# Kernel tuning notes

Hardware: AMD Instinct MI355X
Metric: run time of the kernel (lower is better)

## Reference

```python
import jax, jax.numpy as jnp
import numpy as np
import math

B, S, D_MODEL, N_HEAD, D_HEAD, D_FFN = 1, 2048, 1024, 16, 64, 4096
EPS = 1e-6


def setup_inputs() -> dict:
    key = jax.random.key(0)
    ks = jax.random.split(key, 10)
    scale = 0.02
    x = jax.random.normal(ks[0], (B, S, D_MODEL), dtype=jnp.float32)
    # RoPE frequencies: freqs_cis[s, i] = exp(1j * s * theta_i), theta_i = 10000^{-2i/d_head}
    half = D_HEAD // 2
    inv_freq = 1.0 / (10000.0 ** (jnp.arange(0, half, dtype=jnp.float32) * 2.0 / D_HEAD))
    angles = jnp.arange(S, dtype=jnp.float32)[:, None] * inv_freq[None, :]  # [S, half]
    freqs_cos = jnp.cos(angles)
    freqs_sin = jnp.sin(angles)
    wq = jax.random.normal(ks[1], (D_MODEL, N_HEAD * D_HEAD), dtype=jnp.float32) * scale
    wk = jax.random.normal(ks[2], (D_MODEL, N_HEAD * D_HEAD), dtype=jnp.float32) * scale
    wv = jax.random.normal(ks[3], (D_MODEL, N_HEAD * D_HEAD), dtype=jnp.float32) * scale
    wo = jax.random.normal(ks[4], (N_HEAD * D_HEAD, D_MODEL), dtype=jnp.float32) * scale
    w1 = jax.random.normal(ks[5], (D_MODEL, D_FFN), dtype=jnp.float32) * scale
    w2 = jax.random.normal(ks[6], (D_FFN, D_MODEL), dtype=jnp.float32) * scale
    w3 = jax.random.normal(ks[7], (D_MODEL, D_FFN), dtype=jnp.float32) * scale
    attn_norm_w = jnp.ones((D_MODEL,), dtype=jnp.float32)
    ffn_norm_w = jnp.ones((D_MODEL,), dtype=jnp.float32)
    return {"x": x, "freqs_cos": freqs_cos, "freqs_sin": freqs_sin,
            "wq": wq, "wk": wk, "wv": wv, "wo": wo,
            "w1": w1, "w2": w2, "w3": w3,
            "attn_norm_w": attn_norm_w, "ffn_norm_w": ffn_norm_w}


def _rmsnorm(x, w):
    xf = x.astype(jnp.float32)
    inv = jax.lax.rsqrt(jnp.mean(xf * xf, axis=-1, keepdims=True) + EPS)
    return (xf * inv).astype(x.dtype) * w


def _rope(t, cos, sin):
    # t: [B, S, H, D]; treat last dim as interleaved (even, odd) complex pairs
    b, s, h, d = t.shape
    tr = t.astype(jnp.float32).reshape(b, s, h, d // 2, 2)
    te, to = tr[..., 0], tr[..., 1]
    c = cos[None, :, None, :]
    sn = sin[None, :, None, :]
    out = jnp.stack([te * c - to * sn, te * sn + to * c], axis=-1)
    return out.reshape(b, s, h, d).astype(t.dtype)


def reference(x, freqs_cos, freqs_sin, wq, wk, wv, wo, w1, w2, w3, attn_norm_w, ffn_norm_w):
    bsz, seqlen, _ = x.shape
    # --- attention sub-block ---
    hin = _rmsnorm(x, attn_norm_w)
    q = (hin @ wq).reshape(bsz, seqlen, N_HEAD, D_HEAD)
    k = (hin @ wk).reshape(bsz, seqlen, N_HEAD, D_HEAD)
    v = (hin @ wv).reshape(bsz, seqlen, N_HEAD, D_HEAD)
    q = _rope(q, freqs_cos, freqs_sin)
    k = _rope(k, freqs_cos, freqs_sin)
    # [B, H, S, S] scores, softmax in fp32 (no causal mask in original)
    scores = jnp.einsum('bqhd,bkhd->bhqk', q, k) / math.sqrt(D_HEAD)
    probs = jax.nn.softmax(scores.astype(jnp.float32), axis=-1).astype(q.dtype)
    attn = jnp.einsum('bhqk,bkhd->bqhd', probs, v).reshape(bsz, seqlen, N_HEAD * D_HEAD)
    h = x + attn @ wo
    # --- SwiGLU FFN sub-block ---
    f = _rmsnorm(h, ffn_norm_w)
    ffn = (jax.nn.silu(f @ w1) * (f @ w3)) @ w2
    return h + ffn
```

## Files before the change

kernel.cpp:

```cpp
#include <hip/hip_runtime.h>
#include <stdint.h>
#include <stddef.h>

using bf16x8 = __attribute__((ext_vector_type(8))) __bf16;
using f32x4  = __attribute__((ext_vector_type(4))) float;
using f32x16 = __attribute__((ext_vector_type(16))) float;

__device__ __forceinline__ float bf2f(unsigned short u) {
  union { unsigned int i; float f; } v; v.i = ((unsigned int)u) << 16; return v.f;
}
__device__ __forceinline__ unsigned short f2bf(float f) {
  union { float f; unsigned int i; } v; v.f = f;
  unsigned int r = v.i + 0x7fffu + ((v.i >> 16) & 1u);
  return (unsigned short)(r >> 16);
}
__device__ __forceinline__ unsigned short f2bf_trunc(float f) {
  union { float f; unsigned int i; } v; v.f = f;
  return (unsigned short)(v.i >> 16);
}
__device__ __forceinline__ void async16(const void* g, void* l) {
  __builtin_amdgcn_global_load_lds(
      (const __attribute__((address_space(1))) unsigned int*)g,
      (__attribute__((address_space(3))) unsigned int*)l, 16, 0, 0);
}

#define S_LEN 2048
#define DMODEL 1024
#define NHEAD 16
#define DHEAD 64
#define DFFN 4096

struct T4 {
  const float *s0, *s1, *s2, *s3;
  unsigned short *d0, *d1, *d2, *d3;
};
__global__ __launch_bounds__(256) void transpose4_k(T4 j) {
  const float* in = blockIdx.z == 0 ? j.s0 : blockIdx.z == 1 ? j.s1 : blockIdx.z == 2 ? j.s2 : j.s3;
  unsigned short* out = blockIdx.z == 0 ? j.d0 : blockIdx.z == 1 ? j.d1 : blockIdx.z == 2 ? j.d2 : j.d3;
  __shared__ unsigned short tile[32][33];
  const int tx = threadIdx.x & 31;
  const int ty = threadIdx.x >> 5;
  const int bc = blockIdx.x * 32;
  const int br = blockIdx.y * 32;
#pragma unroll
  for (int i = 0; i < 4; ++i)
    tile[ty + i * 8][tx] = f2bf(in[(size_t)(br + ty + i * 8) * 1024 + bc + tx]);
  __syncthreads();
#pragma unroll
  for (int i = 0; i < 4; ++i)
    out[(size_t)(bc + ty + i * 8) * 1024 + br + tx] = tile[tx][ty + i * 8];
}

__global__ __launch_bounds__(256) void transpose13_k(
    const float* __restrict__ w1, const float* __restrict__ w3,
    unsigned short* __restrict__ out) {
  const float* in = blockIdx.z ? w3 : w1;
  const int rb = blockIdx.z * 32;
  __shared__ unsigned short tile[32][33];
  const int tx = threadIdx.x & 31;
  const int ty = threadIdx.x >> 5;
  const int bc = blockIdx.x * 32;
  const int br = blockIdx.y * 32;
#pragma unroll
  for (int i = 0; i < 4; ++i)
    tile[ty + i * 8][tx] = f2bf(in[(size_t)(br + ty + i * 8) * 4096 + bc + tx]);
  __syncthreads();
#pragma unroll
  for (int i = 0; i < 4; ++i) {
    int c = bc + ty + i * 8;
    int dest = (c >> 5) * 64 + rb + (c & 31);
    out[(size_t)dest * 1024 + br + tx] = tile[tx][ty + i * 8];
  }
}

__global__ __launch_bounds__(256) void transpose_w2_k(
    const float* __restrict__ in, unsigned short* __restrict__ out) {
  __shared__ unsigned short tile[32][33];
  const int tx = threadIdx.x & 31;
  const int ty = threadIdx.x >> 5;
  const int bc = blockIdx.x * 32;
  const int br = blockIdx.y * 32;
#pragma unroll
  for (int i = 0; i < 4; ++i)
    tile[ty + i * 8][tx] = f2bf(in[(size_t)(br + ty + i * 8) * 1024 + bc + tx]);
  __syncthreads();
#pragma unroll
  for (int i = 0; i < 4; ++i)
    out[(size_t)(bc + ty + i * 8) * 4096 + br + tx] = tile[tx][ty + i * 8];
}

__global__ __launch_bounds__(256) void vtrans_k(
    const unsigned short* __restrict__ QKV, unsigned short* __restrict__ VtG) {
  __shared__ unsigned short tile[32][33];
  const int tx = threadIdx.x & 31;
  const int ty = threadIdx.x >> 5;
  const int bc = blockIdx.x * 32;
  const int br = blockIdx.y * 32;
#pragma unroll
  for (int i = 0; i < 4; ++i)
    tile[ty + i * 8][tx] = QKV[(size_t)(br + ty + i * 8) * 3072 + 2048 + bc + tx];
  __syncthreads();
#pragma unroll
  for (int i = 0; i < 4; ++i)
    VtG[(size_t)(bc + ty + i * 8) * 2048 + br + tx] = tile[tx][ty + i * 8];
}

__global__ __launch_bounds__(256) void rmsnorm_k(
    const float* __restrict__ X, const float* __restrict__ W,
    unsigned short* __restrict__ Y) {
  const int row = blockIdx.x;
  const int t = threadIdx.x;
  const int lane = t & 63, w = t >> 6;
  const float* x = X + (size_t)row * DMODEL;
  float xs[4];
  float s = 0.f;
#pragma unroll
  for (int i = 0; i < 4; ++i) {
    xs[i] = x[t * 4 + i];
    s += xs[i] * xs[i];
  }
#pragma unroll
  for (int m = 1; m < 64; m <<= 1) s += __shfl_xor(s, m, 64);
  __shared__ float red[4];
  if (lane == 0) red[w] = s;
  __syncthreads();
  float tot = red[0] + red[1] + red[2] + red[3];
  float inv = rsqrtf(tot * (1.0f / DMODEL) + 1e-6f);
#pragma unroll
  for (int i = 0; i < 4; ++i)
    Y[(size_t)row * DMODEL + t * 4 + i] = f2bf(xs[i] * inv * W[t * 4 + i]);
}

template <int MODE>
__global__ __launch_bounds__(256) void gemm_bt(
    const unsigned short* __restrict__ A, int lda,
    const unsigned short* __restrict__ BT,
    void* __restrict__ Cout,
    int K, int N) {
  __shared__ unsigned short As[128 * 64];
  __shared__ unsigned short Bs[128 * 64];
  const int t = threadIdx.x;
  const int lane = t & 63;
  const int w = t >> 6;
  const int qr = (w >> 1) * 64, qc = (w & 1) * 64;
  const int l31 = lane & 31, half = lane >> 5;
  const int m0 = blockIdx.y * 128, n0 = blockIdx.x * 128;

  f32x16 acc[2][2] = {};

  int srow[4], scol[4];
#pragma unroll
  for (int p = 0; p < 4; ++p) {
    int off = p * 2048 + t * 8;
    int r = off >> 6;
    srow[p] = r;
    scol[p] = (((off >> 3) & 7) ^ (r & 7)) * 8;
  }

  for (int k0 = 0; k0 < K; k0 += 64) {
    __syncthreads();
#pragma unroll
    for (int p = 0; p < 4; ++p) {
      int off = p * 2048 + t * 8;
      async16(A + (size_t)(m0 + srow[p]) * lda + (k0 + scol[p]), &As[off]);
      async16(BT + (size_t)(n0 + srow[p]) * K + (k0 + scol[p]), &Bs[off]);
    }
    __syncthreads();
#pragma unroll
    for (int ks = 0; ks < 4; ++ks) {
      const int ch = ((ks * 2 + half) ^ (l31 & 7)) * 8;
      bf16x8 a0 = *(const bf16x8*)&As[(qr + l31) * 64 + ch];
      bf16x8 a1 = *(const bf16x8*)&As[(qr + 32 + l31) * 64 + ch];
      bf16x8 b0 = *(const bf16x8*)&Bs[(qc + l31) * 64 + ch];
      bf16x8 b1 = *(const bf16x8*)&Bs[(qc + 32 + l31) * 64 + ch];
      acc[0][0] = __builtin_amdgcn_mfma_f32_32x32x16_bf16(a0, b0, acc[0][0], 0, 0, 0);
      acc[0][1] = __builtin_amdgcn_mfma_f32_32x32x16_bf16(a0, b1, acc[0][1], 0, 0, 0);
      acc[1][0] = __builtin_amdgcn_mfma_f32_32x32x16_bf16(a1, b0, acc[1][0], 0, 0, 0);
      acc[1][1] = __builtin_amdgcn_mfma_f32_32x32x16_bf16(a1, b1, acc[1][1], 0, 0, 0);
    }
  }

  {
    unsigned short* C = (unsigned short*)Cout;
#pragma unroll
    for (int rt = 0; rt < 2; ++rt)
#pragma unroll
      for (int ct = 0; ct < 2; ++ct)
#pragma unroll
        for (int reg = 0; reg < 16; ++reg) {
          int rr = m0 + qr + rt * 32 + (reg & 3) + 8 * (reg >> 2) + 4 * half;
          int cc = n0 + qc + ct * 32 + l31;
          C[(size_t)rr * N + cc] = f2bf(acc[rt][ct][reg]);
        }
  }
}

__device__ __forceinline__ void mfma8(f32x16& c0, f32x16& c1,
                                      const bf16x8 (&a)[2][4],
                                      const bf16x8 (&b)[4]) {
  __builtin_amdgcn_s_setprio(1);
#pragma unroll
  for (int ks = 0; ks < 4; ++ks) {
    c0 = __builtin_amdgcn_mfma_f32_32x32x16_bf16(a[0][ks], b[ks], c0, 0, 0, 0);
    c1 = __builtin_amdgcn_mfma_f32_32x32x16_bf16(a[1][ks], b[ks], c1, 0, 0, 0);
  }
  __builtin_amdgcn_s_setprio(0);
}

__global__ __launch_bounds__(512, 2) void gemm256_silu(
    const unsigned short* __restrict__ A,
    const unsigned short* __restrict__ BT,
    unsigned short* __restrict__ F) {
  __shared__ unsigned short lds[65536];
  const int t = threadIdx.x;
  const int l = t & 63, l31 = l & 31, half = l >> 5;
  const int w = t >> 6;
  const int wm = w >> 2, wn = w & 3;

  const int orig = blockIdx.x;
  const int bx = (orig & 7) * 4 + ((orig >> 3) & 3);
  const int by = orig >> 5;
  const int m0 = by * 256, n0 = bx * 256;

  const int rA = t >> 3;
  const int sc = ((t & 7) ^ ((t >> 3) & 7)) * 8;
  const int lo = t * 8;

#define STAGE_A(h, tile, d)                                                    \
  { async16(A + (size_t)(m0 + (h) * 128 + rA) * 1024 + (tile) * 64 + sc,       \
            &lds[(d) * 32768 + (h) * 8192 + lo]);                              \
    async16(A + (size_t)(m0 + (h) * 128 + 64 + rA) * 1024 + (tile) * 64 + sc,  \
            &lds[(d) * 32768 + (h) * 8192 + 4096 + lo]); }
#define STAGE_B(h, tile, d)                                                    \
  { async16(BT + (size_t)(n0 + (h) * 128 + rA) * 1024 + (tile) * 64 + sc,      \
            &lds[(d) * 32768 + 16384 + (h) * 8192 + lo]);                      \
    async16(BT + (size_t)(n0 + (h) * 128 + 64 + rA) * 1024 + (tile) * 64 + sc, \
            &lds[(d) * 32768 + 16384 + (h) * 8192 + 4096 + lo]); }

  const int arow = wm * 128 + l31;
  const int brow = wn * 64 + l31;
  int kc[4];
#pragma unroll
  for (int ks = 0; ks < 4; ++ks) kc[ks] = ((ks * 2 + half) ^ (l31 & 7)) * 8;

#define LDA(d, mt, ks) (*(const bf16x8*)&lds[(d) * 32768 + (arow + (mt) * 32) * 64 + kc[ks]])
#define LDB(d, nt, ks) (*(const bf16x8*)&lds[(d) * 32768 + 16384 + (brow + (nt) * 32) * 64 + kc[ks]])

  f32x16 acc[4][2] = {};
  bf16x8 afr[2][4], bfr[2][4];

  STAGE_A(0, 0, 0); STAGE_A(1, 0, 0); STAGE_B(0, 0, 0); STAGE_B(1, 0, 0);
  STAGE_A(0, 1, 1);
  asm volatile("s_waitcnt vmcnt(2)" ::: "memory");
  __builtin_amdgcn_s_barrier();

#pragma unroll 1
  for (int i = 0; i < 8; ++i) {
    const int t1 = 2 * i + 1, t2 = 2 * i + 2, t3 = 2 * i + 3;
    const bool more = i < 7;

#pragma unroll
    for (int ks = 0; ks < 4; ++ks) {
      afr[0][ks] = LDA(0, 0, ks);
      afr[1][ks] = LDA(0, 1, ks);
      bfr[0][ks] = LDB(0, 0, ks);
    }
    STAGE_A(1, t1, 1);
    __builtin_amdgcn_s_barrier();
    mfma8(acc[0][0], acc[1][0], afr, bfr[0]);
    __builtin_amdgcn_s_barrier();

#pragma unroll
    for (int ks = 0; ks < 4; ++ks) bfr[1][ks] = LDB(0, 1, ks);
    STAGE_B(0, t1, 1);
    __builtin_amdgcn_s_barrier();
    mfma8(acc[0][1], acc[1][1], afr, bfr[1]);
    __builtin_amdgcn_s_barrier();

#pragma unroll
    for (int ks = 0; ks < 4; ++ks) {
      afr[0][ks] = LDA(0, 2, ks);
      afr[1][ks] = LDA(0, 3, ks);
    }
    STAGE_B(1, t1, 1);
    __builtin_amdgcn_s_barrier();
    mfma8(acc[2][1], acc[3][1], afr, bfr[1]);
    __builtin_amdgcn_s_barrier();

    if (more) {
      STAGE_A(0, t2, 0);
      asm volatile("s_waitcnt vmcnt(2)" ::: "memory");
    } else {
      asm volatile("s_waitcnt vmcnt(0)" ::: "memory");
    }
    __builtin_amdgcn_s_barrier();
    mfma8(acc[2][0], acc[3][0], afr, bfr[0]);
    __builtin_amdgcn_s_barrier();

#pragma unroll
    for (int ks = 0; ks < 4; ++ks) {
      afr[0][ks] = LDA(1, 0, ks);
      afr[1][ks] = LDA(1, 1, ks);
      bfr[0][ks] = LDB(1, 0, ks);
    }
    if (more) STAGE_A(1, t2, 0);
    __builtin_amdgcn_s_barrier();
    mfma8(acc[0][0], acc[1][0], afr, bfr[0]);
    __builtin_amdgcn_s_barrier();

#pragma unroll
    for (int ks = 0; ks < 4; ++ks) bfr[1][ks] = LDB(1, 1, ks);
    if (more) STAGE_B(0, t2, 0);
    __builtin_amdgcn_s_barrier();
    mfma8(acc[0][1], acc[1][1], afr, bfr[1]);
    __builtin_amdgcn_s_barrier();

#pragma unroll
    for (int ks = 0; ks < 4; ++ks) {
      afr[0][ks] = LDA(1, 2, ks);
      afr[1][ks] = LDA(1, 3, ks);
    }
    if (more) STAGE_B(1, t2, 0);
    __builtin_amdgcn_s_barrier();
    mfma8(acc[2][1], acc[3][1], afr, bfr[1]);
    __builtin_amdgcn_s_barrier();

    if (more) STAGE_A(0, t3, 1);
    asm volatile("s_waitcnt vmcnt(2)" ::: "memory");
    __builtin_amdgcn_s_barrier();
    mfma8(acc[2][0], acc[3][0], afr, bfr[0]);
    __builtin_amdgcn_s_barrier();
  }

#undef STAGE_A
#undef STAGE_B
#undef LDA
#undef LDB

  const int ccol = (n0 >> 1) + wn * 32 + l31;
  const int rbase = m0 + wm * 128 + 4 * half;
#pragma unroll
  for (int mt = 0; mt < 4; ++mt)
#pragma unroll
    for (int reg = 0; reg < 16; ++reg) {
      int rr = rbase + mt * 32 + (reg & 3) + 8 * (reg >> 2);
      float a1v = acc[mt][0][reg];
      float a3v = acc[mt][1][reg];
      float f = a1v / (1.f + __expf(-a1v)) * a3v;
      F[(size_t)rr * 4096 + ccol] = f2bf(f);
    }
}

struct PtrPair { float* p0; float* p1; };

__global__ __launch_bounds__(256) void gemm_bt_sk(
    const unsigned short* __restrict__ A, int lda,
    const unsigned short* __restrict__ BT,
    PtrPair parts, int Kc, int Ktot, int N) {
  __shared__ unsigned short As[64 * 64];
  __shared__ unsigned short Bs[128 * 64];
  const int t = threadIdx.x;
  const int lane = t & 63;
  const int w = t >> 6;
  const int qr = (w >> 1) * 32, qc = (w & 1) * 64;
  const int l31 = lane & 31, half = lane >> 5;
  const int m0 = blockIdx.y * 64, n0 = blockIdx.x * 128;
  const int kb = blockIdx.z * Kc;

  f32x16 acc[2] = {};

  for (int k0 = 0; k0 < Kc; k0 += 64) {
    __syncthreads();
#pragma unroll
    for (int p = 0; p < 2; ++p) {
      int off = p * 2048 + t * 8;
      int r = off >> 6;
      int sc = (((off >> 3) & 7) ^ (r & 7)) * 8;
      async16(A + (size_t)(m0 + r) * lda + (kb + k0 + sc), &As[off]);
    }
#pragma unroll
    for (int p = 0; p < 4; ++p) {
      int off = p * 2048 + t * 8;
      int r = off >> 6;
      int sc = (((off >> 3) & 7) ^ (r & 7)) * 8;
      async16(BT + (size_t)(n0 + r) * Ktot + (kb + k0 + sc), &Bs[off]);
    }
    __syncthreads();
#pragma unroll
    for (int ks = 0; ks < 4; ++ks) {
      const int ch = ((ks * 2 + half) ^ (l31 & 7)) * 8;
      bf16x8 a0 = *(const bf16x8*)&As[(qr + l31) * 64 + ch];
      bf16x8 b0 = *(const bf16x8*)&Bs[(qc + l31) * 64 + ch];
      bf16x8 b1 = *(const bf16x8*)&Bs[(qc + 32 + l31) * 64 + ch];
      acc[0] = __builtin_amdgcn_mfma_f32_32x32x16_bf16(a0, b0, acc[0], 0, 0, 0);
      acc[1] = __builtin_amdgcn_mfma_f32_32x32x16_bf16(a0, b1, acc[1], 0, 0, 0);
    }
  }

  float* C = blockIdx.z ? parts.p1 : parts.p0;
#pragma unroll
  for (int ct = 0; ct < 2; ++ct)
#pragma unroll
    for (int reg = 0; reg < 16; ++reg) {
      int rr = m0 + qr + (reg & 3) + 8 * (reg >> 2) + 4 * half;
      int cc = n0 + qc + ct * 32 + l31;
      C[(size_t)rr * N + cc] = acc[ct][reg];
    }
}

__global__ __launch_bounds__(256) void reduce2_k(
    const float4* __restrict__ P0, const float4* __restrict__ P1,
    const float4* __restrict__ R, float4* __restrict__ Out, int nvec) {
  int i = blockIdx.x * 256 + threadIdx.x;
  if (i >= nvec) return;
  float4 a = P0[i], b = P1[i], r = R[i];
  float4 o;
  o.x = a.x + b.x + r.x;
  o.y = a.y + b.y + r.y;
  o.z = a.z + b.z + r.z;
  o.w = a.w + b.w + r.w;
  Out[i] = o;
}

__global__ __launch_bounds__(256) void rope_k(
    unsigned short* __restrict__ QKV,
    const float* __restrict__ cosp,
    const float* __restrict__ sinp) {
  int idx = blockIdx.x * 256 + threadIdx.x;
  int s = idx >> 9;
  int rem = idx & 511;
  int h = rem >> 5;
  int i = rem & 31;
  float c = cosp[s * 32 + i];
  float sn = sinp[s * 32 + i];
  size_t off = (size_t)s * 3072 + h * 64 + 2 * i;
  {
    float e = bf2f(QKV[off]), o = bf2f(QKV[off + 1]);
    QKV[off] = f2bf(e * c - o * sn);
    QKV[off + 1] = f2bf(e * sn + o * c);
  }
  {
    float e = bf2f(QKV[off + 1024]), o = bf2f(QKV[off + 1025]);
    QKV[off + 1024] = f2bf((e * c - o * sn) * 0.125f);
    QKV[off + 1025] = f2bf((e * sn + o * c) * 0.125f);
  }
}

#define VPAD 132
__device__ __forceinline__ int swz(int row, int col) { return col ^ ((row & 7) * 8); }

__global__ __launch_bounds__(256) void attn_k(
    const unsigned short* __restrict__ QKV,
    const unsigned short* __restrict__ VtG,
    float* __restrict__ O0, float* __restrict__ O1,
    float* __restrict__ L) {
  const int h = blockIdx.y;
  const int qb = blockIdx.x;
  const int z = blockIdx.z;
  const int t = threadIdx.x;
  const int lane = t & 63;
  const int w = t >> 6;
  const int row16 = lane & 15, quad = lane >> 4;
  const int q0 = qb * 64 + w * 16;
  const int kbase = z * 1024;

  __shared__ unsigned short Ks[128 * 64];
  __shared__ unsigned short Vt[64 * 128];
  __shared__ unsigned short Ps[4][16 * VPAD];

  const unsigned short* Qp = QKV;
  const unsigned short* Kp = QKV + 1024;
  const unsigned short* Vg = VtG + (size_t)h * 64 * 2048;

  bf16x8 aq[2];
#pragma unroll
  for (int kk = 0; kk < 2; ++kk)
    aq[kk] = *(const bf16x8*)(Qp + (size_t)(q0 + row16) * 3072 + h * 64 + kk * 32 + quad * 8);

  f32x4 o[4] = {};
  float l_r[4] = {0.f, 0.f, 0.f, 0.f};

  bf16x8 kreg[4], vreg[4];
#pragma unroll
  for (int p = 0; p < 4; ++p) {
    int off = p * 2048 + t * 8;
    int r = off >> 6, c = off & 63;
    kreg[p] = *(const bf16x8*)(Kp + (size_t)(kbase + r) * 3072 + h * 64 + c);
    int d = off >> 7, key = off & 127;
    vreg[p] = *(const bf16x8*)(Vg + (size_t)d * 2048 + kbase + key);
  }

  for (int kb = kbase; kb < kbase + 1024; kb += 128) {
    __syncthreads();
#pragma unroll
    for (int p = 0; p < 4; ++p) {
      int off = p * 2048 + t * 8;
      int r = off >> 6, c = off & 63;
      *(bf16x8*)&Ks[r * 64 + swz(r, c)] = kreg[p];
      int d = off >> 7, key = off & 127;
      *(bf16x8*)&Vt[d * 128 + swz(d, key)] = vreg[p];
    }
    __syncthreads();
    if (kb + 128 < kbase + 1024) {
      int kb2 = kb + 128;
#pragma unroll
      for (int p = 0; p < 4; ++p) {
        int off = p * 2048 + t * 8;
        int r = off >> 6, c = off & 63;
        kreg[p] = *(const bf16x8*)(Kp + (size_t)(kb2 + r) * 3072 + h * 64 + c);
        int d = off >> 7, key = off & 127;
        vreg[p] = *(const bf16x8*)(Vg + (size_t)d * 2048 + kb2 + key);
      }
    }

    f32x4 sc[8];
#pragma unroll
    for (int tj = 0; tj < 8; ++tj) {
      int kr = tj * 16 + row16;
      bf16x8 b0 = *(const bf16x8*)&Ks[kr * 64 + swz(kr, quad * 8)];
      bf16x8 b1 = *(const bf16x8*)&Ks[kr * 64 + swz(kr, 32 + quad * 8)];
      f32x4 z4 = {};
      z4 = __builtin_amdgcn_mfma_f32_16x16x32_bf16(aq[0], b0, z4, 0, 0, 0);
      z4 = __builtin_amdgcn_mfma_f32_16x16x32_bf16(aq[1], b1, z4, 0, 0, 0);
      sc[tj] = z4;
    }

#pragma unroll
    for (int reg = 0; reg < 4; ++reg) {
      float ssum = 0.f;
#pragma unroll
      for (int tj = 0; tj < 8; ++tj) {
        float p = __expf(sc[tj][reg]);
        sc[tj][reg] = p;
        ssum += p;
      }
#pragma unroll
      for (int m = 1; m < 16; m <<= 1) ssum += __shfl_xor(ssum, m, 16);
      l_r[reg] += ssum;
    }

#pragma unroll
    for (int tj = 0; tj < 8; ++tj)
#pragma unroll
      for (int reg = 0; reg < 4; ++reg)
        Ps[w][(quad * 4 + reg) * VPAD + tj * 16 + row16] = f2bf_trunc(sc[tj][reg]);

    bf16x8 ap[4];
#pragma unroll
    for (int kk = 0; kk < 4; ++kk)
      ap[kk] = *(const bf16x8*)&Ps[w][row16 * VPAD + kk * 32 + quad * 8];
#pragma unroll
    for (int dt = 0; dt < 4; ++dt) {
      int dr = dt * 16 + row16;
#pragma unroll
      for (int kk = 0; kk < 4; ++kk) {
        bf16x8 bv = *(const bf16x8*)&Vt[dr * 128 + swz(dr, kk * 32 + quad * 8)];
        o[dt] = __builtin_amdgcn_mfma_f32_16x16x32_bf16(ap[kk], bv, o[dt], 0, 0, 0);
      }
    }
  }

  float* Op = z ? O1 : O0;
#pragma unroll
  for (int dt = 0; dt < 4; ++dt)
#pragma unroll
    for (int reg = 0; reg < 4; ++reg)
      Op[(size_t)(q0 + quad * 4 + reg) * DMODEL + h * 64 + dt * 16 + row16] = o[dt][reg];
  if (row16 == 0)
#pragma unroll
    for (int reg = 0; reg < 4; ++reg)
      L[(size_t)(h * 2 + z) * S_LEN + q0 + quad * 4 + reg] = l_r[reg];
}

__global__ __launch_bounds__(256) void attn_combine_k(
    const float4* __restrict__ O0, const float4* __restrict__ O1,
    const float* __restrict__ L, unsigned short* __restrict__ Attn) {
  int i = blockIdx.x * 256 + threadIdx.x;
  int e0 = i * 4;
  int s = e0 >> 10;
  int c = e0 & 1023;
  int h = c >> 6;
  float la = L[(size_t)(h * 2) * S_LEN + s];
  float lb = L[(size_t)(h * 2 + 1) * S_LEN + s];
  float inv = 1.f / (la + lb);
  float4 a = O0[i], b = O1[i];
  ushort4 r;
  r.x = f2bf((a.x + b.x) * inv);
  r.y = f2bf((a.y + b.y) * inv);
  r.z = f2bf((a.z + b.z) * inv);
  r.w = f2bf((a.w + b.w) * inv);
  *(ushort4*)(Attn + e0) = r;
}

extern "C" void kernel_launch(void* const* d_in, const int* in_sizes, int n_in,
                              void* d_out, int out_size, void* d_ws, size_t ws_size,
                              hipStream_t stream) {
  (void)in_sizes; (void)n_in; (void)out_size; (void)ws_size;
  const float* x    = (const float*)d_in[0];
  const float* fcos = (const float*)d_in[1];
  const float* fsin = (const float*)d_in[2];
  const float* wq   = (const float*)d_in[3];
  const float* wk   = (const float*)d_in[4];
  const float* wv   = (const float*)d_in[5];
  const float* wo   = (const float*)d_in[6];
  const float* w1   = (const float*)d_in[7];
  const float* w2   = (const float*)d_in[8];
  const float* w3   = (const float*)d_in[9];
  const float* anw  = (const float*)d_in[10];
  const float* fnw  = (const float*)d_in[11];
  float* out = (float*)d_out;
  char* ws = (char*)d_ws;

  unsigned short* WqkvT = (unsigned short*)(ws + 0);
  unsigned short* VtG   = (unsigned short*)(ws + 0);
  float*          Lbuf  = (float*)(ws + 4194304);
  unsigned short* WoT   = (unsigned short*)(ws + 6291456);
  unsigned short* QKV   = (unsigned short*)(ws + 8388608);
  unsigned short* Attn  = (unsigned short*)(ws + 20971520);
  float* Oa             = (float*)(ws + 25165824);
  float* Ob             = (float*)(ws + 37748736);
  float* P0a            = (float*)(ws + 8388608);
  float* P1a            = (float*)(ws + 25165824);
  unsigned short* F     = (unsigned short*)(ws + 0);
  float* P0b            = (float*)(ws + 16777216);
  float* P1b            = (float*)(ws + 25165824);
  unsigned short* Hin   = (unsigned short*)(ws + 33554432);
  float*          Hres  = (float*)        (ws + 37748736);
  unsigned short* W13I  = (unsigned short*)(ws + 46137344);
  unsigned short* W2T   = (unsigned short*)(ws + 62914560);

  transpose4_k<<<dim3(32, 32, 4), 256, 0, stream>>>(
      T4{wq, wk, wv, wo, WqkvT, WqkvT + 1048576, WqkvT + 2097152, WoT});
  transpose13_k<<<dim3(128, 32, 2), 256, 0, stream>>>(w1, w3, W13I);
  transpose_w2_k<<<dim3(32, 128), 256, 0, stream>>>(w2, W2T);

  rmsnorm_k<<<2048, 256, 0, stream>>>(x, anw, Hin);
  gemm_bt<0><<<dim3(24, 16), 256, 0, stream>>>(Hin, 1024, WqkvT, QKV, 1024, 3072);
  rope_k<<<4096, 256, 0, stream>>>(QKV, fcos, fsin);
  vtrans_k<<<dim3(32, 64), 256, 0, stream>>>(QKV, VtG);
  attn_k<<<dim3(32, 16, 2), 256, 0, stream>>>(QKV, VtG, Oa, Ob, Lbuf);
  attn_combine_k<<<2048, 256, 0, stream>>>((const float4*)Oa, (const float4*)Ob, Lbuf, Attn);
  gemm_bt_sk<<<dim3(8, 32, 2), 256, 0, stream>>>(Attn, 1024, WoT, PtrPair{P0a, P1a}, 512, 1024, 1024);
  reduce2_k<<<2048, 256, 0, stream>>>((const float4*)P0a, (const float4*)P1a,
                                      (const float4*)x, (float4*)Hres, 524288);

  rmsnorm_k<<<2048, 256, 0, stream>>>(Hres, fnw, Hin);
  gemm256_silu<<<dim3(256), 512, 0, stream>>>(Hin, W13I, F);
  gemm_bt_sk<<<dim3(8, 32, 2), 256, 0, stream>>>(F, 4096, W2T, PtrPair{P0b, P1b}, 2048, 4096, 1024);
  reduce2_k<<<2048, 256, 0, stream>>>((const float4*)P0b, (const float4*)P1b,
                                      (const float4*)Hres, (float4*)out, 524288);
}
```

Before: 309.4 us.

## Rewrite attention with 32x32 MFMA and async double-buffered K/V; reorder GEMM prefetch

The attention kernel now gives each wave 32 queries and uses 32x32x16 bf16 MFMA to compute transposed scores (K·Q). Probabilities are repacked into MFMA A-fragments in registers with cross-half shuffles instead of a round trip through LDS. K and V tiles are loaded with async global-to-LDS copies into double buffers with an XOR swizzle, and the grid is halved. Separately, the pipelined 256-tile GEMM reorders its A/B stage issues and vmcnt waits to prefetch further ahead, which keeps more loads in flight but is more fragile to get right.

```diff
diff --git a/kernel.cpp b/kernel.cpp
--- a/kernel.cpp
+++ b/kernel.cpp
@@ -17,6 +17,15 @@
 __device__ __forceinline__ unsigned short f2bf_trunc(float f) {
   union { float f; unsigned int i; } v; v.f = f;
   return (unsigned short)(v.i >> 16);
+}
+__device__ __forceinline__ unsigned int pk_trunc(float a, float b) {
+  union { float f; unsigned int i; } x, y; x.f = a; y.f = b;
+  return (x.i >> 16) | (y.i & 0xffff0000u);
+}
+__device__ __forceinline__ bf16x8 mk_bf16x8(unsigned int a, unsigned int b,
+                                            unsigned int c, unsigned int d) {
+  union { unsigned int u[4]; bf16x8 v; } x;
+  x.u[0] = a; x.u[1] = b; x.u[2] = c; x.u[3] = d; return x.v;
 }
 __device__ __forceinline__ void async16(const void* g, void* l) {
   __builtin_amdgcn_global_load_lds(
@@ -250,8 +259,8 @@
   bf16x8 afr[2][4], bfr[2][4];
 
   STAGE_A(0, 0, 0); STAGE_A(1, 0, 0); STAGE_B(0, 0, 0); STAGE_B(1, 0, 0);
-  STAGE_A(0, 1, 1);
-  asm volatile("s_waitcnt vmcnt(2)" ::: "memory");
+  STAGE_A(0, 1, 1); STAGE_A(1, 1, 1);
+  asm volatile("s_waitcnt vmcnt(4)" ::: "memory");
   __builtin_amdgcn_s_barrier();
 
 #pragma unroll 1
@@ -265,14 +274,14 @@
       afr[1][ks] = LDA(0, 1, ks);
       bfr[0][ks] = LDB(0, 0, ks);
     }
-    STAGE_A(1, t1, 1);
+    STAGE_B(0, t1, 1);
     __builtin_amdgcn_s_barrier();
     mfma8(acc[0][0], acc[1][0], afr, bfr[0]);
     __builtin_amdgcn_s_barrier();
 
 #pragma unroll
     for (int ks = 0; ks < 4; ++ks) bfr[1][ks] = LDB(0, 1, ks);
-    STAGE_B(0, t1, 1);
+    STAGE_B(1, t1, 1);
     __builtin_amdgcn_s_barrier();
     mfma8(acc[0][1], acc[1][1], afr, bfr[1]);
     __builtin_amdgcn_s_barrier();
@@ -282,16 +291,17 @@
       afr[0][ks] = LDA(0, 2, ks);
       afr[1][ks] = LDA(0, 3, ks);
     }
-    STAGE_B(1, t1, 1);
+    if (more) STAGE_B(0, t2, 0);
     __builtin_amdgcn_s_barrier();
     mfma8(acc[2][1], acc[3][1], afr, bfr[1]);
     __builtin_amdgcn_s_barrier();
 
     if (more) {
+      STAGE_B(1, t2, 0);
       STAGE_A(0, t2, 0);
+      asm volatile("s_waitcnt vmcnt(8)" ::: "memory");
+    } else {
       asm volatile("s_waitcnt vmcnt(2)" ::: "memory");
-    } else {
-      asm volatile("s_waitcnt vmcnt(0)" ::: "memory");
     }
     __builtin_amdgcn_s_barrier();
     mfma8(acc[2][0], acc[3][0], afr, bfr[0]);
@@ -303,14 +313,18 @@
       afr[1][ks] = LDA(1, 1, ks);
       bfr[0][ks] = LDB(1, 0, ks);
     }
-    if (more) STAGE_A(1, t2, 0);
+    if (more) {
+      STAGE_A(1, t2, 0);
+      asm volatile("s_waitcnt vmcnt(8)" ::: "memory");
+    } else {
+      asm volatile("s_waitcnt vmcnt(0)" ::: "memory");
+    }
     __builtin_amdgcn_s_barrier();
     mfma8(acc[0][0], acc[1][0], afr, bfr[0]);
     __builtin_amdgcn_s_barrier();
 
 #pragma unroll
     for (int ks = 0; ks < 4; ++ks) bfr[1][ks] = LDB(1, 1, ks);
-    if (more) STAGE_B(0, t2, 0);
     __builtin_amdgcn_s_barrier();
     mfma8(acc[0][1], acc[1][1], afr, bfr[1]);
     __builtin_amdgcn_s_barrier();
@@ -320,13 +334,17 @@
       afr[0][ks] = LDA(1, 2, ks);
       afr[1][ks] = LDA(1, 3, ks);
     }
-    if (more) STAGE_B(1, t2, 0);
     __builtin_amdgcn_s_barrier();
     mfma8(acc[2][1], acc[3][1], afr, bfr[1]);
     __builtin_amdgcn_s_barrier();
 
-    if (more) STAGE_A(0, t3, 1);
-    asm volatile("s_waitcnt vmcnt(2)" ::: "memory");
+    if (more) {
+      STAGE_A(0, t3, 1);
+      STAGE_A(1, t3, 1);
+      asm volatile("s_waitcnt vmcnt(4)" ::: "memory");
+    } else {
+      asm volatile("s_waitcnt vmcnt(0)" ::: "memory");
+    }
     __builtin_amdgcn_s_barrier();
     mfma8(acc[2][0], acc[3][0], afr, bfr[0]);
     __builtin_amdgcn_s_barrier();
@@ -446,9 +464,6 @@
   }
 }
 
-#define VPAD 132
-__device__ __forceinline__ int swz(int row, int col) { return col ^ ((row & 7) * 8); }
-
 __global__ __launch_bounds__(256) void attn_k(
     const unsigned short* __restrict__ QKV,
     const unsigned short* __restrict__ VtG,
@@ -459,117 +474,115 @@
   const int z = blockIdx.z;
   const int t = threadIdx.x;
   const int lane = t & 63;
+  const int l31 = lane & 31, half = lane >> 5;
   const int w = t >> 6;
-  const int row16 = lane & 15, quad = lane >> 4;
-  const int q0 = qb * 64 + w * 16;
+  const int q0 = qb * 128 + w * 32;
   const int kbase = z * 1024;
 
-  __shared__ unsigned short Ks[128 * 64];
-  __shared__ unsigned short Vt[64 * 128];
-  __shared__ unsigned short Ps[4][16 * VPAD];
-
-  const unsigned short* Qp = QKV;
-  const unsigned short* Kp = QKV + 1024;
+  __shared__ unsigned short Kt[2][64 * 64];
+  __shared__ unsigned short Vt[2][64 * 64];
+
+  const unsigned short* Kp = QKV + 1024 + h * 64;
   const unsigned short* Vg = VtG + (size_t)h * 64 * 2048;
 
-  bf16x8 aq[2];
-#pragma unroll
-  for (int kk = 0; kk < 2; ++kk)
-    aq[kk] = *(const bf16x8*)(Qp + (size_t)(q0 + row16) * 3072 + h * 64 + kk * 32 + quad * 8);
-
-  f32x4 o[4] = {};
-  float l_r[4] = {0.f, 0.f, 0.f, 0.f};
-
-  bf16x8 kreg[4], vreg[4];
-#pragma unroll
-  for (int p = 0; p < 4; ++p) {
+  bf16x8 qf[4];
+#pragma unroll
+  for (int ks = 0; ks < 4; ++ks)
+    qf[ks] = *(const bf16x8*)(QKV + (size_t)(q0 + l31) * 3072 + h * 64 + ks * 16 + half * 8);
+
+#pragma unroll
+  for (int p = 0; p < 2; ++p) {
     int off = p * 2048 + t * 8;
-    int r = off >> 6, c = off & 63;
-    kreg[p] = *(const bf16x8*)(Kp + (size_t)(kbase + r) * 3072 + h * 64 + c);
-    int d = off >> 7, key = off & 127;
-    vreg[p] = *(const bf16x8*)(Vg + (size_t)d * 2048 + kbase + key);
-  }
-
-  for (int kb = kbase; kb < kbase + 1024; kb += 128) {
+    int r = off >> 6;
+    int sc8 = (((off >> 3) & 7) ^ (r & 7)) * 8;
+    async16(Kp + (size_t)(kbase + r) * 3072 + sc8, &Kt[0][off]);
+    async16(Vg + (size_t)r * 2048 + kbase + sc8, &Vt[0][off]);
+  }
+  asm volatile("s_waitcnt vmcnt(0)" ::: "memory");
+  __syncthreads();
+
+  f32x16 oacc[2] = {};
+  float l_r = 0.f;
+
+#pragma unroll 1
+  for (int kt = 0; kt < 16; ++kt) {
+    const int cur = kt & 1;
+    if (kt + 1 < 16) {
+      int kb2 = kbase + (kt + 1) * 64;
+#pragma unroll
+      for (int p = 0; p < 2; ++p) {
+        int off = p * 2048 + t * 8;
+        int r = off >> 6;
+        int sc8 = (((off >> 3) & 7) ^ (r & 7)) * 8;
+        async16(Kp + (size_t)(kb2 + r) * 3072 + sc8, &Kt[cur ^ 1][off]);
+        async16(Vg + (size_t)r * 2048 + kb2 + sc8, &Vt[cur ^ 1][off]);
+      }
+    }
+
+    f32x16 st[2] = {};
+#pragma unroll
+    for (int ks = 0; ks < 4; ++ks) {
+      const int ch = ((2 * ks + half) ^ (l31 & 7)) * 8;
+      bf16x8 k0 = *(const bf16x8*)&Kt[cur][l31 * 64 + ch];
+      bf16x8 k1 = *(const bf16x8*)&Kt[cur][(32 + l31) * 64 + ch];
+      st[0] = __builtin_amdgcn_mfma_f32_32x32x16_bf16(k0, qf[ks], st[0], 0, 0, 0);
+      st[1] = __builtin_amdgcn_mfma_f32_32x32x16_bf16(k1, qf[ks], st[1], 0, 0, 0);
+    }
+
+    float psum = 0.f;
+#pragma unroll
+    for (int b = 0; b < 2; ++b)
+#pragma unroll
+      for (int r = 0; r < 16; ++r) {
+        float e = __expf(st[b][r]);
+        st[b][r] = e;
+        psum += e;
+      }
+    l_r += psum;
+
+    unsigned int pklo[8], pkhi[8];
+#pragma unroll
+    for (int b = 0; b < 2; ++b)
+#pragma unroll
+      for (int m = 0; m < 4; ++m) {
+        pklo[b * 4 + m] = pk_trunc(st[b][4 * m + 0], st[b][4 * m + 1]);
+        pkhi[b * 4 + m] = pk_trunc(st[b][4 * m + 2], st[b][4 * m + 3]);
+      }
+
+#pragma unroll
+    for (int ks = 0; ks < 4; ++ks) {
+      unsigned int keep_lo = half ? pklo[2 * ks + 1] : pklo[2 * ks];
+      unsigned int keep_hi = half ? pkhi[2 * ks + 1] : pkhi[2 * ks];
+      unsigned int pass_lo = half ? pklo[2 * ks] : pklo[2 * ks + 1];
+      unsigned int pass_hi = half ? pkhi[2 * ks] : pkhi[2 * ks + 1];
+      unsigned int olo = (unsigned int)__shfl_xor((int)pass_lo, 32, 64);
+      unsigned int ohi = (unsigned int)__shfl_xor((int)pass_hi, 32, 64);
+      unsigned int w0 = half ? olo : keep_lo;
+      unsigned int w1 = half ? ohi : keep_hi;
+      unsigned int w2 = half ? keep_lo : olo;
+      unsigned int w3 = half ? keep_hi : ohi;
+      bf16x8 af = mk_bf16x8(w0, w1, w2, w3);
+      const int ch = ((2 * ks + half) ^ (l31 & 7)) * 8;
+      bf16x8 v0 = *(const bf16x8*)&Vt[cur][l31 * 64 + ch];
+      bf16x8 v1 = *(const bf16x8*)&Vt[cur][(32 + l31) * 64 + ch];
+      oacc[0] = __builtin_amdgcn_mfma_f32_32x32x16_bf16(af, v0, oacc[0], 0, 0, 0);
+      oacc[1] = __builtin_amdgcn_mfma_f32_32x32x16_bf16(af, v1, oacc[1], 0, 0, 0);
+    }
+
     __syncthreads();
-#pragma unroll
-    for (int p = 0; p < 4; ++p) {
-      int off = p * 2048 + t * 8;
-      int r = off >> 6, c = off & 63;
-      *(bf16x8*)&Ks[r * 64 + swz(r, c)] = kreg[p];
-      int d = off >> 7, key = off & 127;
-      *(bf16x8*)&Vt[d * 128 + swz(d, key)] = vreg[p];
-    }
-    __syncthreads();
-    if (kb + 128 < kbase + 1024) {
-      int kb2 = kb + 128;
-#pragma unroll
-      for (int p = 0; p < 4; ++p) {
-        int off = p * 2048 + t * 8;
-        int r = off >> 6, c = off & 63;
-        kreg[p] = *(const bf16x8*)(Kp + (size_t)(kb2 + r) * 3072 + h * 64 + c);
-        int d = off >> 7, key = off & 127;
-        vreg[p] = *(const bf16x8*)(Vg + (size_t)d * 2048 + kb2 + key);
-      }
-    }
-
-    f32x4 sc[8];
-#pragma unroll
-    for (int tj = 0; tj < 8; ++tj) {
-      int kr = tj * 16 + row16;
-      bf16x8 b0 = *(const bf16x8*)&Ks[kr * 64 + swz(kr, quad * 8)];
-      bf16x8 b1 = *(const bf16x8*)&Ks[kr * 64 + swz(kr, 32 + quad * 8)];
-      f32x4 z4 = {};
-      z4 = __builtin_amdgcn_mfma_f32_16x16x32_bf16(aq[0], b0, z4, 0, 0, 0);
-      z4 = __builtin_amdgcn_mfma_f32_16x16x32_bf16(aq[1], b1, z4, 0, 0, 0);
-      sc[tj] = z4;
-    }
-
-#pragma unroll
-    for (int reg = 0; reg < 4; ++reg) {
-      float ssum = 0.f;
-#pragma unroll
-      for (int tj = 0; tj < 8; ++tj) {
-        float p = __expf(sc[tj][reg]);
-        sc[tj][reg] = p;
-        ssum += p;
-      }
-#pragma unroll
-      for (int m = 1; m < 16; m <<= 1) ssum += __shfl_xor(ssum, m, 16);
-      l_r[reg] += ssum;
-    }
-
-#pragma unroll
-    for (int tj = 0; tj < 8; ++tj)
-#pragma unroll
-      for (int reg = 0; reg < 4; ++reg)
-        Ps[w][(quad * 4 + reg) * VPAD + tj * 16 + row16] = f2bf_trunc(sc[tj][reg]);
-
-    bf16x8 ap[4];
-#pragma unroll
-    for (int kk = 0; kk < 4; ++kk)
-      ap[kk] = *(const bf16x8*)&Ps[w][row16 * VPAD + kk * 32 + quad * 8];
-#pragma unroll
-    for (int dt = 0; dt < 4; ++dt) {
-      int dr = dt * 16 + row16;
-#pragma unroll
-      for (int kk = 0; kk < 4; ++kk) {
-        bf16x8 bv = *(const bf16x8*)&Vt[dr * 128 + swz(dr, kk * 32 + quad * 8)];
-        o[dt] = __builtin_amdgcn_mfma_f32_16x16x32_bf16(ap[kk], bv, o[dt], 0, 0, 0);
-      }
-    }
-  }
-
+  }
+
+  float lt = l_r + __shfl_xor(l_r, 32, 64);
   float* Op = z ? O1 : O0;
 #pragma unroll
-  for (int dt = 0; dt < 4; ++dt)
-#pragma unroll
-    for (int reg = 0; reg < 4; ++reg)
-      Op[(size_t)(q0 + quad * 4 + reg) * DMODEL + h * 64 + dt * 16 + row16] = o[dt][reg];
-  if (row16 == 0)
-#pragma unroll
-    for (int reg = 0; reg < 4; ++reg)
-      L[(size_t)(h * 2 + z) * S_LEN + q0 + quad * 4 + reg] = l_r[reg];
+  for (int db = 0; db < 2; ++db)
+#pragma unroll
+    for (int reg = 0; reg < 16; ++reg) {
+      int q = (reg & 3) + 8 * (reg >> 2) + 4 * half;
+      Op[(size_t)(q0 + q) * DMODEL + h * 64 + db * 32 + l31] = oacc[db][reg];
+    }
+  if (half == 0)
+    L[(size_t)(h * 2 + z) * S_LEN + q0 + l31] = lt;
 }
 
 __global__ __launch_bounds__(256) void attn_combine_k(
@@ -638,7 +651,7 @@
   gemm_bt<0><<<dim3(24, 16), 256, 0, stream>>>(Hin, 1024, WqkvT, QKV, 1024, 3072);
   rope_k<<<4096, 256, 0, stream>>>(QKV, fcos, fsin);
   vtrans_k<<<dim3(32, 64), 256, 0, stream>>>(QKV, VtG);
-  attn_k<<<dim3(32, 16, 2), 256, 0, stream>>>(QKV, VtG, Oa, Ob, Lbuf);
+  attn_k<<<dim3(16, 16, 2), 256, 0, stream>>>(QKV, VtG, Oa, Ob, Lbuf);
   attn_combine_k<<<2048, 256, 0, stream>>>((const float4*)Oa, (const float4*)Ob, Lbuf, Attn);
   gemm_bt_sk<<<dim3(8, 32, 2), 256, 0, stream>>>(Attn, 1024, WoT, PtrPair{P0a, P1a}, 512, 1024, 1024);
   reduce2_k<<<2048, 256, 0, stream>>>((const float4*)P0a, (const float4*)P1a,
```

After: 299.1 us. 3.3% less time.
